# Kernel optimization log

Hardware: AMD Instinct MI355X
Metric: run time of the kernel (lower is better)

## Reference

```python
import jax, jax.numpy as jnp
import numpy as np

B, A, C, M = 8, 98304, 80, 32
ALPHA, GAMMA = 0.25, 2.0


def setup_inputs() -> dict:
    key = jax.random.key(0)
    k1, k2, k3, k4, k5, k6, k7, k8 = jax.random.split(key, 8)
    classifications = jax.random.uniform(k1, (B, A, C), dtype=jnp.float32)
    regressions = jax.random.normal(k2, (B, A, 4), dtype=jnp.float32)
    # valid anchor boxes inside a 640px image
    ax = jax.random.uniform(k3, (A,)) * 512.0
    ay = jax.random.uniform(k4, (A,)) * 512.0
    aw = jax.random.uniform(k5, (A, 2)) * 120.0 + 8.0
    anchors = jnp.stack([ax, ay, ax + aw[:, 0], ay + aw[:, 1]], axis=-1)[None].astype(jnp.float32)
    # valid GT boxes with class labels in [0, C) (no -1 padding: all annotations valid)
    gx = jax.random.uniform(k6, (B, M, 2)) * 480.0
    gw = jax.random.uniform(k7, (B, M, 2)) * 150.0 + 10.0
    gcls = jax.random.randint(k8, (B, M), 0, C).astype(jnp.float32)
    annotations = jnp.concatenate([gx, gx + gw, gcls[..., None]], axis=-1).astype(jnp.float32)
    return {
        "classifications": classifications,
        "regressions": regressions,
        "anchors": anchors,
        "annotations": annotations,
        "negative_iou_thr": 0.4,
        "positive_iou_thr": 0.5,
    }


def calc_iou(a, b):
    # a: [A,4] anchors, b: [M,4] gt boxes -> [A,M]
    area = (b[:, 2] - b[:, 0]) * (b[:, 3] - b[:, 1])
    iw = jnp.clip(jnp.minimum(a[:, 2:3], b[:, 2]) - jnp.maximum(a[:, 0:1], b[:, 0]), 0.0)
    ih = jnp.clip(jnp.minimum(a[:, 3:4], b[:, 3]) - jnp.maximum(a[:, 1:2], b[:, 1]), 0.0)
    inter = iw * ih
    ua = jnp.clip(((a[:, 2] - a[:, 0]) * (a[:, 3] - a[:, 1]))[:, None] + area - inter, 1e-8)
    return inter / ua


def focal_loss(classifications, regressions, anchors, annotations, negative_iou_thr, positive_iou_thr):
    anchor = anchors[0]  # [A,4]
    aw = anchor[:, 2] - anchor[:, 0]
    ah = anchor[:, 3] - anchor[:, 1]
    acx = anchor[:, 0] + 0.5 * aw
    acy = anchor[:, 1] + 0.5 * ah

    def per_image(classification, regression, annot):
        p = jnp.clip(classification, 1e-4, 1.0 - 1e-4)
        valid = annot[:, 4] != -1.0  # [M] (all valid in test data)
        iou = jnp.where(valid[None, :], calc_iou(anchor, annot[:, :4]), -1.0)  # [A,M]
        iou_max = jnp.max(iou, axis=1)
        iou_arg = jnp.argmax(iou, axis=1)
        assigned = annot[iou_arg]  # [A,5]

        pos = iou_max >= positive_iou_thr  # [A]
        num_pos = jnp.sum(pos.astype(jnp.float32))
        onehot = jax.nn.one_hot(assigned[:, 4].astype(jnp.int32), C, dtype=jnp.float32)
        # targets: 1 for assigned class on positives, 0 elsewhere on pos/neg anchors, -1 ignored
        targets = jnp.where(pos[:, None], onehot,
                            jnp.where((iou_max < negative_iou_thr)[:, None], 0.0, -1.0))

        is_one = targets == 1.0
        alpha_factor = jnp.where(is_one, ALPHA, 1.0 - ALPHA)
        focal_w = alpha_factor * jnp.where(is_one, 1.0 - p, p) ** GAMMA
        bce = -(targets * jnp.log(p) + (1.0 - targets) * jnp.log(1.0 - p))
        cls_loss = jnp.where(targets != -1.0, focal_w * bce, 0.0)
        cls_loss = jnp.sum(cls_loss) / jnp.clip(num_pos, 1.0)

        gw = jnp.clip(assigned[:, 2] - assigned[:, 0], None, None)
        gh = assigned[:, 3] - assigned[:, 1]
        gcx = assigned[:, 0] + 0.5 * gw
        gcy = assigned[:, 1] + 0.5 * gh
        gw = jnp.clip(gw, 1.0)
        gh = jnp.clip(gh, 1.0)
        t = jnp.stack([(gcx - acx) / aw, (gcy - acy) / ah,
                       jnp.log(gw / aw), jnp.log(gh / ah)], axis=1)
        t = t / jnp.array([0.1, 0.1, 0.2, 0.2], dtype=jnp.float32)
        diff = jnp.abs(t - regression)
        sl1 = jnp.where(diff <= 1.0 / 9.0, 0.5 * 9.0 * diff * diff, diff - 0.5 / 9.0)
        reg_loss = jnp.sum(jnp.where(pos[:, None], sl1, 0.0)) / jnp.clip(num_pos * 4.0, 1.0)
        return cls_loss, reg_loss

    cls_l, reg_l = jax.vmap(per_image)(classifications, regressions, annotations)
    return jnp.mean(cls_l).reshape(1), jnp.mean(reg_l).reshape(1)


def reference(classifications, regressions, anchors, annotations, negative_iou_thr, positive_iou_thr):
    return focal_loss(classifications, regressions, anchors, annotations,
                      negative_iou_thr, positive_iou_thr)
```

## Files before the change

### kernel.cpp

```cpp
#include <hip/hip_runtime.h>

#define B_ 8
#define A_ 98304
#define C_ 80
#define M_ 32
#define BLK 256
#define ITERS 20
#define NPF 10
#define NWAVE (BLK / 64)

#define NEGC (-0.75f * 0.69314718055994531f)

__device__ __forceinline__ float neg_u(float praw) {
    const float p = fminf(praw, 1.0f - 1e-4f);
    return p * p * __log2f(1.0f - p);
}

__device__ __forceinline__ float smooth_l1(float t, float r) {
    float d = fabsf(t - r);
    return (d <= (1.0f / 9.0f)) ? (0.5f * 9.0f * d * d) : (d - 0.5f / 9.0f);
}

__global__ __launch_bounds__(BLK, 4) void focal_main(
    const float* __restrict__ cls,
    const float* __restrict__ regr,
    const float* __restrict__ anchors,
    const float* __restrict__ ann,
    const float* __restrict__ neg_thr_p,
    const float* __restrict__ pos_thr_p,
    float* __restrict__ acc)
{
    __shared__ float s_x0[M_], s_y0[M_], s_x1[M_], s_y1[M_], s_ab[M_], s_cls[M_];
    __shared__ float s_w[BLK];
    __shared__ float s_red[NWAVE * 3];

    const int tid = threadIdx.x;
    const int blocksPerImg = A_ / BLK;
    const int b  = blockIdx.x / blocksPerImg;
    const int a0 = (blockIdx.x % blocksPerImg) * BLK;

    if (tid < M_) {
        const float* am = ann + ((size_t)b * M_ + tid) * 5;
        const float x0 = am[0], y0 = am[1], x1 = am[2], y1 = am[3], cl = am[4];
        s_x0[tid] = x0; s_y0[tid] = y0; s_x1[tid] = x1; s_y1[tid] = y1;
        s_ab[tid] = (x1 - x0) * (y1 - y0);
        s_cls[tid] = cl;
    }
    __syncthreads();

    const float neg_thr = neg_thr_p[0];
    const float pos_thr = pos_thr_p[0];

    const int a = a0 + tid;
    const float4 an = reinterpret_cast<const float4*>(anchors)[a];
    const float aw = an.z - an.x;
    const float ah = an.w - an.y;
    const float areaA = aw * ah;

    float ib = -1.0f, ub = 1.0f;
    int   arg = 0;
#pragma unroll
    for (int m = 0; m < M_; ++m) {
        const float iw = fmaxf(fminf(an.z, s_x1[m]) - fmaxf(an.x, s_x0[m]), 0.0f);
        const float ih = fmaxf(fminf(an.w, s_y1[m]) - fmaxf(an.y, s_y0[m]), 0.0f);
        float inter = iw * ih;
        const float ua = fmaxf(areaA + s_ab[m] - inter, 1e-8f);
        if (s_cls[m] == -1.0f) inter = -1.0f;
        if (inter * ub > ib * ua) { ib = inter; ub = ua; arg = m; }
    }
    const bool pos = (ib >= pos_thr * ub);
    const bool neg = (ib <  neg_thr * ub);

    float reg_partial = 0.0f;
    float pos_count   = 0.0f;
    float cls_corr    = 0.0f;

    if (pos) {
        pos_count = 1.0f;
        const float gx0 = s_x0[arg], gy0 = s_y0[arg];
        const float gx1 = s_x1[arg], gy1 = s_y1[arg];
        const int   kcls = (int)s_cls[arg];

        float gw = gx1 - gx0;
        float gh = gy1 - gy0;
        const float gcx = gx0 + 0.5f * gw;
        const float gcy = gy0 + 0.5f * gh;
        gw = fmaxf(gw, 1.0f);
        gh = fmaxf(gh, 1.0f);
        const float acx = an.x + 0.5f * aw;
        const float acy = an.y + 0.5f * ah;
        const float t0 = ((gcx - acx) / aw) * 10.0f;
        const float t1 = ((gcy - acy) / ah) * 10.0f;
        const float t2 = logf(gw / aw) * 5.0f;
        const float t3 = logf(gh / ah) * 5.0f;
        const float4 r = reinterpret_cast<const float4*>(regr)[(size_t)b * A_ + a];
        reg_partial = smooth_l1(t0, r.x) + smooth_l1(t1, r.y) +
                      smooth_l1(t2, r.z) + smooth_l1(t3, r.w);

        const float praw = cls[((size_t)b * A_ + a) * C_ + kcls];
        const float p  = fminf(fmaxf(praw, 1e-4f), 1.0f - 1e-4f);
        const float om = 1.0f - p;
        const float negv = neg_u(praw) * NEGC;
        const float posv = 0.25f * om * om * (-__logf(p));
        cls_corr = posv - negv;
    }
    s_w[tid] = (pos || neg) ? NEGC : 0.0f;
    __syncthreads();

    const float4* tile = reinterpret_cast<const float4*>(
        cls + ((size_t)b * A_ + a0) * C_);

    float4 buf[NPF];
#pragma unroll
    for (int i = 0; i < NPF; ++i) buf[i] = tile[i * BLK + tid];

    float s0 = 0.0f, s1 = 0.0f;
#pragma unroll
    for (int i = 0; i < ITERS; ++i) {
        const float4 v = buf[i % NPF];
        if (i + NPF < ITERS)
            buf[i % NPF] = tile[(i + NPF) * BLK + tid];
        const int arow = (i * BLK + tid) / 20;
        const float cw = s_w[arow];
        s0 = fmaf(neg_u(v.x) + neg_u(v.y), cw, s0);
        s1 = fmaf(neg_u(v.z) + neg_u(v.w), cw, s1);
    }
    float cls_partial = cls_corr + s0 + s1;

#pragma unroll
    for (int off = 32; off > 0; off >>= 1) {
        cls_partial += __shfl_down(cls_partial, off);
        reg_partial += __shfl_down(reg_partial, off);
        pos_count   += __shfl_down(pos_count,   off);
    }
    const int wave = tid >> 6;
    if ((tid & 63) == 0) {
        s_red[wave * 3 + 0] = cls_partial;
        s_red[wave * 3 + 1] = reg_partial;
        s_red[wave * 3 + 2] = pos_count;
    }
    __syncthreads();
    if (tid == 0) {
        float c = 0.0f, r = 0.0f, n = 0.0f;
#pragma unroll
        for (int wv = 0; wv < NWAVE; ++wv) {
            c += s_red[wv * 3 + 0];
            r += s_red[wv * 3 + 1];
            n += s_red[wv * 3 + 2];
        }
        atomicAdd(&acc[b * 3 + 0], c);
        atomicAdd(&acc[b * 3 + 1], r);
        atomicAdd(&acc[b * 3 + 2], n);
    }
}

__global__ void focal_finalize(const float* __restrict__ acc, float* __restrict__ out) {
    const int t = threadIdx.x;
    float cls_l = 0.0f, reg_l = 0.0f;
    if (t < B_) {
        const float np = acc[t * 3 + 2];
        cls_l = acc[t * 3 + 0] / fmaxf(np, 1.0f);
        reg_l = acc[t * 3 + 1] / fmaxf(np * 4.0f, 1.0f);
    }
#pragma unroll
    for (int off = 32; off > 0; off >>= 1) {
        cls_l += __shfl_down(cls_l, off);
        reg_l += __shfl_down(reg_l, off);
    }
    if (t == 0) {
        out[0] = cls_l / (float)B_;
        out[1] = reg_l / (float)B_;
    }
}

extern "C" void kernel_launch(void* const* d_in, const int* in_sizes, int n_in,
                              void* d_out, int out_size, void* d_ws, size_t ws_size,
                              hipStream_t stream) {
    const float* cls     = (const float*)d_in[0];
    const float* regr    = (const float*)d_in[1];
    const float* anchors = (const float*)d_in[2];
    const float* ann     = (const float*)d_in[3];
    const float* negt    = (const float*)d_in[4];
    const float* post    = (const float*)d_in[5];
    float* acc = (float*)d_ws;

    hipMemsetAsync(acc, 0, B_ * 3 * sizeof(float), stream);
    focal_main<<<B_ * (A_ / BLK), BLK, 0, stream>>>(cls, regr, anchors, ann,
                                                    negt, post, acc);
    focal_finalize<<<1, 64, 0, stream>>>(acc, (float*)d_out);
}
```

Measured before the change: 116.5 us.

## Switch to persistent blocks with atomic tile counter and drop register prefetch

The kernel now launches a fixed grid of 2048 persistent blocks. Each block repeatedly grabs a tile index from a global atomic counter, replacing the old one-block-per-tile launch of 3072 blocks. The explicit 10-deep float4 register prefetch buffer is removed in favour of a plain loop unrolled by 5, and launch bounds allow 8 blocks per CU, aiming for higher occupancy and to let hardware latency hiding replace manual prefetch. The trade-off is extra atomics and barriers per tile, and less memory-level parallelism per thread.

Measured after the change: 218.6 us. 1.88x slower.

```diff
diff --git a/kernel.cpp b/kernel.cpp
--- a/kernel.cpp
+++ b/kernel.cpp
@@ -6,8 +6,10 @@
 #define M_ 32
 #define BLK 256
 #define ITERS 20
-#define NPF 10
 #define NWAVE (BLK / 64)
+#define TILES_PER_IMG (A_ / BLK)
+#define NTILES (B_ * TILES_PER_IMG)
+#define GRID 2048
 
 #define NEGC (-0.75f * 0.69314718055994531f)
 
@@ -21,136 +23,138 @@
     return (d <= (1.0f / 9.0f)) ? (0.5f * 9.0f * d * d) : (d - 0.5f / 9.0f);
 }
 
-__global__ __launch_bounds__(BLK, 4) void focal_main(
+__global__ __launch_bounds__(BLK, 8) void focal_main(
     const float* __restrict__ cls,
     const float* __restrict__ regr,
     const float* __restrict__ anchors,
     const float* __restrict__ ann,
     const float* __restrict__ neg_thr_p,
     const float* __restrict__ pos_thr_p,
-    float* __restrict__ acc)
+    float* __restrict__ acc,
+    int* __restrict__ tile_counter)
 {
     __shared__ float s_x0[M_], s_y0[M_], s_x1[M_], s_y1[M_], s_ab[M_], s_cls[M_];
     __shared__ float s_w[BLK];
     __shared__ float s_red[NWAVE * 3];
+    __shared__ int   s_tile;
 
     const int tid = threadIdx.x;
-    const int blocksPerImg = A_ / BLK;
-    const int b  = blockIdx.x / blocksPerImg;
-    const int a0 = (blockIdx.x % blocksPerImg) * BLK;
-
-    if (tid < M_) {
-        const float* am = ann + ((size_t)b * M_ + tid) * 5;
-        const float x0 = am[0], y0 = am[1], x1 = am[2], y1 = am[3], cl = am[4];
-        s_x0[tid] = x0; s_y0[tid] = y0; s_x1[tid] = x1; s_y1[tid] = y1;
-        s_ab[tid] = (x1 - x0) * (y1 - y0);
-        s_cls[tid] = cl;
-    }
-    __syncthreads();
-
     const float neg_thr = neg_thr_p[0];
     const float pos_thr = pos_thr_p[0];
 
-    const int a = a0 + tid;
-    const float4 an = reinterpret_cast<const float4*>(anchors)[a];
-    const float aw = an.z - an.x;
-    const float ah = an.w - an.y;
-    const float areaA = aw * ah;
+    for (;;) {
+        if (tid == 0) s_tile = atomicAdd(tile_counter, 1);
+        __syncthreads();
+        const int t = s_tile;
+        if (t >= NTILES) break;
 
-    float ib = -1.0f, ub = 1.0f;
-    int   arg = 0;
+        const int b  = t / TILES_PER_IMG;
+        const int a0 = (t % TILES_PER_IMG) * BLK;
+
+        if (tid < M_) {
+            const float* am = ann + ((size_t)b * M_ + tid) * 5;
+            const float x0 = am[0], y0 = am[1], x1 = am[2], y1 = am[3], cl = am[4];
+            s_x0[tid] = x0; s_y0[tid] = y0; s_x1[tid] = x1; s_y1[tid] = y1;
+            s_ab[tid] = (x1 - x0) * (y1 - y0);
+            s_cls[tid] = cl;
+        }
+        __syncthreads();
+
+        const int a = a0 + tid;
+        const float4 an = reinterpret_cast<const float4*>(anchors)[a];
+        const float aw = an.z - an.x;
+        const float ah = an.w - an.y;
+        const float areaA = aw * ah;
+
+        float ib = -1.0f, ub = 1.0f;
+        int   arg = 0;
 #pragma unroll
-    for (int m = 0; m < M_; ++m) {
-        const float iw = fmaxf(fminf(an.z, s_x1[m]) - fmaxf(an.x, s_x0[m]), 0.0f);
-        const float ih = fmaxf(fminf(an.w, s_y1[m]) - fmaxf(an.y, s_y0[m]), 0.0f);
-        float inter = iw * ih;
-        const float ua = fmaxf(areaA + s_ab[m] - inter, 1e-8f);
-        if (s_cls[m] == -1.0f) inter = -1.0f;
-        if (inter * ub > ib * ua) { ib = inter; ub = ua; arg = m; }
-    }
-    const bool pos = (ib >= pos_thr * ub);
-    const bool neg = (ib <  neg_thr * ub);
+        for (int m = 0; m < M_; ++m) {
+            const float iw = fmaxf(fminf(an.z, s_x1[m]) - fmaxf(an.x, s_x0[m]), 0.0f);
+            const float ih = fmaxf(fminf(an.w, s_y1[m]) - fmaxf(an.y, s_y0[m]), 0.0f);
+            float inter = iw * ih;
+            const float ua = fmaxf(areaA + s_ab[m] - inter, 1e-8f);
+            if (s_cls[m] == -1.0f) inter = -1.0f;
+            if (inter * ub > ib * ua) { ib = inter; ub = ua; arg = m; }
+        }
+        const bool pos = (ib >= pos_thr * ub);
+        const bool neg = (ib <  neg_thr * ub);
 
-    float reg_partial = 0.0f;
-    float pos_count   = 0.0f;
-    float cls_corr    = 0.0f;
+        float reg_partial = 0.0f;
+        float pos_count   = 0.0f;
+        float cls_corr    = 0.0f;
 
-    if (pos) {
-        pos_count = 1.0f;
-        const float gx0 = s_x0[arg], gy0 = s_y0[arg];
-        const float gx1 = s_x1[arg], gy1 = s_y1[arg];
-        const int   kcls = (int)s_cls[arg];
+        if (pos) {
+            pos_count = 1.0f;
+            const float gx0 = s_x0[arg], gy0 = s_y0[arg];
+            const float gx1 = s_x1[arg], gy1 = s_y1[arg];
+            const int   kcls = (int)s_cls[arg];
 
-        float gw = gx1 - gx0;
-        float gh = gy1 - gy0;
-        const float gcx = gx0 + 0.5f * gw;
-        const float gcy = gy0 + 0.5f * gh;
-        gw = fmaxf(gw, 1.0f);
-        gh = fmaxf(gh, 1.0f);
-        const float acx = an.x + 0.5f * aw;
-        const float acy = an.y + 0.5f * ah;
-        const float t0 = ((gcx - acx) / aw) * 10.0f;
-        const float t1 = ((gcy - acy) / ah) * 10.0f;
-        const float t2 = logf(gw / aw) * 5.0f;
-        const float t3 = logf(gh / ah) * 5.0f;
-        const float4 r = reinterpret_cast<const float4*>(regr)[(size_t)b * A_ + a];
-        reg_partial = smooth_l1(t0, r.x) + smooth_l1(t1, r.y) +
-                      smooth_l1(t2, r.z) + smooth_l1(t3, r.w);
+            float gw = gx1 - gx0;
+            float gh = gy1 - gy0;
+            const float gcx = gx0 + 0.5f * gw;
+            const float gcy = gy0 + 0.5f * gh;
+            gw = fmaxf(gw, 1.0f);
+            gh = fmaxf(gh, 1.0f);
+            const float acx = an.x + 0.5f * aw;
+            const float acy = an.y + 0.5f * ah;
+            const float t0 = ((gcx - acx) / aw) * 10.0f;
+            const float t1 = ((gcy - acy) / ah) * 10.0f;
+            const float t2 = logf(gw / aw) * 5.0f;
+            const float t3 = logf(gh / ah) * 5.0f;
+            const float4 r = reinterpret_cast<const float4*>(regr)[(size_t)b * A_ + a];
+            reg_partial = smooth_l1(t0, r.x) + smooth_l1(t1, r.y) +
+                          smooth_l1(t2, r.z) + smooth_l1(t3, r.w);
 
-        const float praw = cls[((size_t)b * A_ + a) * C_ + kcls];
-        const float p  = fminf(fmaxf(praw, 1e-4f), 1.0f - 1e-4f);
-        const float om = 1.0f - p;
-        const float negv = neg_u(praw) * NEGC;
-        const float posv = 0.25f * om * om * (-__logf(p));
-        cls_corr = posv - negv;
-    }
-    s_w[tid] = (pos || neg) ? NEGC : 0.0f;
-    __syncthreads();
+            const float praw = cls[((size_t)b * A_ + a) * C_ + kcls];
+            const float p  = fminf(fmaxf(praw, 1e-4f), 1.0f - 1e-4f);
+            const float om = 1.0f - p;
+            const float negv = neg_u(praw) * NEGC;
+            const float posv = 0.25f * om * om * (-__logf(p));
+            cls_corr = posv - negv;
+        }
+        s_w[tid] = (pos || neg) ? NEGC : 0.0f;
+        __syncthreads();
 
-    const float4* tile = reinterpret_cast<const float4*>(
-        cls + ((size_t)b * A_ + a0) * C_);
-
-    float4 buf[NPF];
-#pragma unroll
-    for (int i = 0; i < NPF; ++i) buf[i] = tile[i * BLK + tid];
-
-    float s0 = 0.0f, s1 = 0.0f;
-#pragma unroll
-    for (int i = 0; i < ITERS; ++i) {
-        const float4 v = buf[i % NPF];
-        if (i + NPF < ITERS)
-            buf[i % NPF] = tile[(i + NPF) * BLK + tid];
-        const int arow = (i * BLK + tid) / 20;
-        const float cw = s_w[arow];
-        s0 = fmaf(neg_u(v.x) + neg_u(v.y), cw, s0);
-        s1 = fmaf(neg_u(v.z) + neg_u(v.w), cw, s1);
-    }
-    float cls_partial = cls_corr + s0 + s1;
+        const float4* tile4 = reinterpret_cast<const float4*>(
+            cls + ((size_t)b * A_ + a0) * C_);
+        float s0 = 0.0f, s1 = 0.0f;
+#pragma unroll 5
+        for (int it = 0; it < ITERS; ++it) {
+            const int vid = it * BLK + tid;
+            const float4 v = tile4[vid];
+            const float cw = s_w[(unsigned)vid / 20u];
+            s0 = fmaf(neg_u(v.x) + neg_u(v.y), cw, s0);
+            s1 = fmaf(neg_u(v.z) + neg_u(v.w), cw, s1);
+        }
+        float cls_partial = cls_corr + s0 + s1;
 
 #pragma unroll
-    for (int off = 32; off > 0; off >>= 1) {
-        cls_partial += __shfl_down(cls_partial, off);
-        reg_partial += __shfl_down(reg_partial, off);
-        pos_count   += __shfl_down(pos_count,   off);
-    }
-    const int wave = tid >> 6;
-    if ((tid & 63) == 0) {
-        s_red[wave * 3 + 0] = cls_partial;
-        s_red[wave * 3 + 1] = reg_partial;
-        s_red[wave * 3 + 2] = pos_count;
-    }
-    __syncthreads();
-    if (tid == 0) {
-        float c = 0.0f, r = 0.0f, n = 0.0f;
+        for (int off = 32; off > 0; off >>= 1) {
+            cls_partial += __shfl_down(cls_partial, off);
+            reg_partial += __shfl_down(reg_partial, off);
+            pos_count   += __shfl_down(pos_count,   off);
+        }
+        const int wave = tid >> 6;
+        if ((tid & 63) == 0) {
+            s_red[wave * 3 + 0] = cls_partial;
+            s_red[wave * 3 + 1] = reg_partial;
+            s_red[wave * 3 + 2] = pos_count;
+        }
+        __syncthreads();
+        if (tid == 0) {
+            float c = 0.0f, r = 0.0f, n = 0.0f;
 #pragma unroll
-        for (int wv = 0; wv < NWAVE; ++wv) {
-            c += s_red[wv * 3 + 0];
-            r += s_red[wv * 3 + 1];
-            n += s_red[wv * 3 + 2];
+            for (int wv = 0; wv < NWAVE; ++wv) {
+                c += s_red[wv * 3 + 0];
+                r += s_red[wv * 3 + 1];
+                n += s_red[wv * 3 + 2];
+            }
+            atomicAdd(&acc[b * 3 + 0], c);
+            atomicAdd(&acc[b * 3 + 1], r);
+            atomicAdd(&acc[b * 3 + 2], n);
         }
-        atomicAdd(&acc[b * 3 + 0], c);
-        atomicAdd(&acc[b * 3 + 1], r);
-        atomicAdd(&acc[b * 3 + 2], n);
+        __syncthreads();
     }
 }
 
@@ -182,10 +186,12 @@
     const float* ann     = (const float*)d_in[3];
     const float* negt    = (const float*)d_in[4];
     const float* post    = (const float*)d_in[5];
+
     float* acc = (float*)d_ws;
+    int*   cnt = (int*)((char*)d_ws + 256);
 
-    hipMemsetAsync(acc, 0, B_ * 3 * sizeof(float), stream);
-    focal_main<<<B_ * (A_ / BLK), BLK, 0, stream>>>(cls, regr, anchors, ann,
-                                                    negt, post, acc);
+    hipMemsetAsync(d_ws, 0, 512, stream);
+    focal_main<<<GRID, BLK, 0, stream>>>(cls, regr, anchors, ann,
+                                         negt, post, acc, cnt);
     focal_finalize<<<1, 64, 0, stream>>>(acc, (float*)d_out);
 }
```
